# Kernel optimization log

Measured on AMD Instinct MI355X. Metric: run time of the kernel, lower is better.

The kernel has to match this reference:

```python
import jax, jax.numpy as jnp
import numpy as np

N_NODES = 50000
N_GRAPHS = 512
EPS = 1e-5


def _ln(x, g, b):
    mu = jnp.mean(x, axis=-1, keepdims=True)
    var = jnp.var(x, axis=-1, keepdims=True)
    return (x - mu) * jax.lax.rsqrt(var + EPS) * g + b


def _sage(x, src, dst, wl, wr, bl):
    # mean-aggregate neighbor features: messages x[src] -> dst
    s = jax.ops.segment_sum(x[src], dst, num_segments=N_NODES)
    cnt = jax.ops.segment_sum(jnp.ones((src.shape[0],), x.dtype), dst, num_segments=N_NODES)
    agg = s / jnp.maximum(cnt, 1.0)[:, None]
    # PyG SAGEConv: lin_l(agg) + lin_r(x), bias only on lin_l
    return agg @ wl + bl + x @ wr


def setup_inputs() -> dict:
    key = jax.random.key(0)
    ks = jax.random.split(key, 16)
    C, H, NC, E = 128, 128, 2, 800000
    inp = {
        'x': jax.random.normal(ks[0], (N_NODES, C), jnp.float32),
        'edge_index': jax.random.randint(ks[1], (2, E), 0, N_NODES, jnp.int32),
        'batch': jnp.sort(jax.random.randint(ks[2], (N_NODES,), 0, N_GRAPHS, jnp.int32)),
    }
    def w(k, shape):
        return jax.random.normal(k, shape, jnp.float32) * 0.05
    inp.update({
        'w1l': w(ks[3], (C, H)), 'w1r': w(ks[4], (C, H)), 'b1': jnp.zeros((H,), jnp.float32),
        'g1': jnp.ones((H,), jnp.float32), 'be1': jnp.zeros((H,), jnp.float32),
        'w2l': w(ks[5], (H, H)), 'w2r': w(ks[6], (H, H)), 'b2': jnp.zeros((H,), jnp.float32),
        'g2': jnp.ones((H,), jnp.float32), 'be2': jnp.zeros((H,), jnp.float32),
        'w3l': w(ks[7], (H, H)), 'w3r': w(ks[8], (H, H)), 'b3': jnp.zeros((H,), jnp.float32),
        'g3': jnp.ones((H,), jnp.float32), 'be3': jnp.zeros((H,), jnp.float32),
        'wc': w(ks[9], (H, NC)), 'bc': jnp.zeros((NC,), jnp.float32),
    })
    return inp


def reference(x, edge_index, batch, w1l, w1r, b1, g1, be1, w2l, w2r, b2, g2, be2,
              w3l, w3r, b3, g3, be3, wc, bc):
    src, dst = edge_index[0], edge_index[1]
    # eval mode: dropout is identity
    h1 = _ln(jax.nn.relu(_sage(x, src, dst, w1l, w1r, b1)), g1, be1)
    h2 = _ln(jax.nn.relu(_sage(h1, src, dst, w2l, w2r, b2)) + h1, g2, be2)
    h3 = _ln(h2 + jax.nn.relu(_sage(h2, src, dst, w3l, w3r, b3)), g3, be3)
    # global mean pool over graphs
    s = jax.ops.segment_sum(h3, batch, num_segments=N_GRAPHS)
    cnt = jax.ops.segment_sum(jnp.ones((h3.shape[0],), h3.dtype), batch, num_segments=N_GRAPHS)
    avg = s / jnp.maximum(cnt, 1.0)[:, None]
    out = avg @ wc + bc
    return (out, h3, avg)
```

## Files before the change

kernel.cpp:

```cpp
#include <hip/hip_runtime.h>

#define NND 50000
#define NE  800000
#define CF  128
#define NGR 512
#define DCAP 64

typedef __bf16 bf16;
typedef __bf16 bf16x2 __attribute__((ext_vector_type(2)));
typedef __bf16 bf16x4 __attribute__((ext_vector_type(4)));
typedef __bf16 bf16x8 __attribute__((ext_vector_type(8)));
typedef float  f32x4  __attribute__((ext_vector_type(4)));

__device__ __forceinline__ int swz(int n, int k) {
  return n * 256 + (((k >> 3) ^ (n & 31)) << 3) + (k & 7);
}

__global__ __launch_bounds__(256) void conv_k(const float* __restrict__ x,
                                              bf16* __restrict__ xb,
                                              const float* __restrict__ w1l, const float* __restrict__ w1r,
                                              const float* __restrict__ w2l, const float* __restrict__ w2r,
                                              const float* __restrict__ w3l, const float* __restrict__ w3r,
                                              bf16* __restrict__ wb,
                                              const int* __restrict__ batch,
                                              int* __restrict__ gs,
                                              int* __restrict__ cnt) {
  int t = blockIdx.x * 256 + threadIdx.x;
  if (t < (NND * CF / 4)) {
    f32x4 v = ((const f32x4*)x)[t];
    bf16x4 o;
    o[0] = (bf16)v[0]; o[1] = (bf16)v[1]; o[2] = (bf16)v[2]; o[3] = (bf16)v[3];
    ((bf16x4*)xb)[t] = o;
  }
  if (t < 49152) {
    int m = t >> 13, w = t & 8191;
    const float* src = (m == 0) ? w1l : (m == 1) ? w1r : (m == 2) ? w2l
                     : (m == 3) ? w2r : (m == 4) ? w3l : w3r;
    float2 v = *(const float2*)(src + w * 2);
    bf16x2 o;
    o[0] = (bf16)v.x; o[1] = (bf16)v.y;
    ((bf16x2*)wb)[t] = o;
  }
  if (t < NND) {
    cnt[t] = 0;
    int b = batch[t];
    if (t == 0) {
      for (int g = 0; g <= b; g++) gs[g] = 0;
    } else {
      int pb = batch[t - 1];
      for (int g = pb + 1; g <= b; g++) gs[g] = t;
    }
    if (t == NND - 1) {
      for (int g = b + 1; g <= NGR; g++) gs[g] = NND;
    }
  }
}

__global__ __launch_bounds__(256) void fill_k(const int* __restrict__ src,
                                              const int* __restrict__ dst,
                                              int* __restrict__ cnt,
                                              unsigned short* __restrict__ csr) {
  int r  = blockIdx.x & 7;
  int lo = r * 6250, hi = lo + 6250;
  int base = (blockIdx.x >> 3) * 2048;
  int end  = min(base + 2048, NE);
  for (int e = base + threadIdx.x; e < end; e += 256) {
    int d = dst[e];
    if (d >= lo && d < hi) {
      int p = atomicAdd(&cnt[d], 1);
      if (p < DCAP) csr[d * DCAP + p] = (unsigned short)src[e];
    }
  }
}

__global__ __launch_bounds__(256) void agg_k(const bf16* __restrict__ xin,
                                             const int* __restrict__ cnt,
                                             const unsigned short* __restrict__ csr,
                                             bf16* __restrict__ aggout) {
  int wid  = (blockIdx.x * 256 + threadIdx.x) >> 6;
  int lane = threadIdx.x & 63;
  if (wid >= NND) return;
  int sub = lane >> 4;
  int c8  = (lane & 15) * 8;
  int deg = min(cnt[wid], DCAP);
  int ebase = wid * DCAP;
  float a[8] = {};
  for (int e = 0; e < deg; e += 16) {
    int   s[4];
    float m[4];
#pragma unroll
    for (int u = 0; u < 4; u++) {
      int i = e + u * 4 + sub;
      s[u] = csr[ebase + ((i < deg) ? i : 0)];
      m[u] = (i < deg) ? 1.f : 0.f;
    }
    bf16x8 v[4];
#pragma unroll
    for (int u = 0; u < 4; u++) v[u] = *(const bf16x8*)(xin + s[u] * 128 + c8);
#pragma unroll
    for (int u = 0; u < 4; u++)
#pragma unroll
      for (int j = 0; j < 8; j++) a[j] += m[u] * (float)v[u][j];
  }
#pragma unroll
  for (int j = 0; j < 8; j++) {
    a[j] += __shfl_xor(a[j], 16);
    a[j] += __shfl_xor(a[j], 32);
  }
  if (sub == 0) {
    float inv = 1.0f / fmaxf((float)deg, 1.0f);
    bf16x8 o;
#pragma unroll
    for (int j = 0; j < 8; j++) o[j] = (bf16)(a[j] * inv);
    *(bf16x8*)(aggout + wid * 128 + c8) = o;
  }
}

template <typename TO>
__global__ __launch_bounds__(256, 2) void gemm_k(
    const bf16* __restrict__ aggp, const bf16* __restrict__ prev,
    const bf16* __restrict__ wl, const bf16* __restrict__ wr,
    const float* __restrict__ bias, const float* __restrict__ gamma,
    const float* __restrict__ beta, TO* __restrict__ outp, int addres) {
  __shared__ bf16 bt[128 * 256];
  int tid = threadIdx.x;
  for (int e = tid; e < 128 * 64; e += 256) {
    int k  = e >> 6;
    int n2 = (e & 63) << 1;
    {
      bf16x2 v = *(const bf16x2*)(wl + k * 128 + n2);
      bt[swz(n2, k)]     = v[0];
      bt[swz(n2 + 1, k)] = v[1];
    }
    {
      bf16x2 v = *(const bf16x2*)(wr + k * 128 + n2);
      bt[swz(n2, k + 128)]     = v[0];
      bt[swz(n2 + 1, k + 128)] = v[1];
    }
  }
  __syncthreads();

  int wave = tid >> 6, lane = tid & 63;
  int q = lane >> 4, r = lane & 15;
  int wrow = blockIdx.x * 128 + wave * 32;

  int arow[2];
#pragma unroll
  for (int rt = 0; rt < 2; rt++) {
    int ar = wrow + rt * 16 + r;
    arow[rt] = (ar < NND) ? ar : (NND - 1);
  }

  f32x4 acc[2][8] = {};

#pragma unroll
  for (int kk = 0; kk < 8; kk++) {
    int kof = kk * 32 + q * 8;
    bf16x8 af[2];
#pragma unroll
    for (int rt = 0; rt < 2; rt++) {
      const bf16* ap = (kk < 4) ? (aggp + arow[rt] * 128 + kof)
                                : (prev + arow[rt] * 128 + (kof - 128));
      af[rt] = *(const bf16x8*)ap;
    }
#pragma unroll
    for (int t = 0; t < 8; t++) {
      int n = t * 16 + r;
      bf16x8 bfrag = *(const bf16x8*)&bt[n * 256 + (((kof >> 3) ^ (n & 31)) << 3)];
#pragma unroll
      for (int rt = 0; rt < 2; rt++)
        acc[rt][t] = __builtin_amdgcn_mfma_f32_16x16x32_bf16(af[rt], bfrag, acc[rt][t], 0, 0, 0);
    }
  }

  float biasf[8], gf[8], bef[8];
#pragma unroll
  for (int t = 0; t < 8; t++) {
    int c = t * 16 + r;
    biasf[t] = bias[c];
    gf[t]    = gamma[c];
    bef[t]   = beta[c];
  }

#pragma unroll
  for (int rt = 0; rt < 2; rt++) {
#pragma unroll
    for (int reg = 0; reg < 4; reg++) {
      int row = wrow + rt * 16 + q * 4 + reg;
      int rr  = (row < NND) ? row : (NND - 1);
      const bf16* prow = prev + rr * 128;
      float vals[8];
      float s = 0.f, s2 = 0.f;
#pragma unroll
      for (int t = 0; t < 8; t++) {
        float v = acc[rt][t][reg] + biasf[t];
        v = fmaxf(v, 0.f);
        if (addres) v += (float)prow[t * 16 + r];
        vals[t] = v;
        s += v;
        s2 += v * v;
      }
#pragma unroll
      for (int m = 1; m < 16; m <<= 1) {
        s  += __shfl_xor(s, m);
        s2 += __shfl_xor(s2, m);
      }
      float mean = s * (1.f / 128.f);
      float var  = fmaxf(s2 * (1.f / 128.f) - mean * mean, 0.f);
      float rstd = rsqrtf(var + 1e-5f);
      if (row < NND) {
        TO* orow = outp + row * 128;
#pragma unroll
        for (int t = 0; t < 8; t++)
          orow[t * 16 + r] = (TO)((vals[t] - mean) * rstd * gf[t] + bef[t]);
      }
    }
  }
}

__global__ __launch_bounds__(256) void poolhead_k(
    const float* __restrict__ h3, const int* __restrict__ gs,
    const float* __restrict__ wc, const float* __restrict__ bc,
    float* __restrict__ outv, float* __restrict__ avgv) {
  int g = blockIdx.x;
  int s = gs[g], epos = gs[g + 1];
  int tid = threadIdx.x;
  int wave = tid >> 6, lane = tid & 63;
  float a0 = 0.f, a1 = 0.f;
  for (int row = s + wave; row < epos; row += 4) {
    float2 v = *(const float2*)(h3 + row * 128 + 2 * lane);
    a0 += v.x; a1 += v.y;
  }
  __shared__ float red[4][128];
  red[wave][2 * lane]     = a0;
  red[wave][2 * lane + 1] = a1;
  __syncthreads();
  __shared__ float sp[4];
  if (tid < 128) {
    float t4  = red[0][tid] + red[1][tid] + red[2][tid] + red[3][tid];
    float inv = 1.f / fmaxf((float)(epos - s), 1.f);
    float avg = t4 * inv;
    avgv[g * 128 + tid] = avg;
    float p0 = avg * wc[tid * 2 + 0];
    float p1 = avg * wc[tid * 2 + 1];
#pragma unroll
    for (int m = 1; m < 64; m <<= 1) {
      p0 += __shfl_xor(p0, m);
      p1 += __shfl_xor(p1, m);
    }
    if ((tid & 63) == 0) {
      sp[(tid >> 6) * 2]     = p0;
      sp[(tid >> 6) * 2 + 1] = p1;
    }
  }
  __syncthreads();
  if (tid == 0) {
    outv[g * 2 + 0] = sp[0] + sp[2] + bc[0];
    outv[g * 2 + 1] = sp[1] + sp[3] + bc[1];
  }
}

extern "C" void kernel_launch(void* const* d_in, const int* in_sizes, int n_in,
                              void* d_out, int out_size, void* d_ws, size_t ws_size,
                              hipStream_t stream) {
  const float* x   = (const float*)d_in[0];
  const int* ei    = (const int*)d_in[1];
  const int* batch = (const int*)d_in[2];
  const float* w1l = (const float*)d_in[3],  *w1r = (const float*)d_in[4];
  const float* b1  = (const float*)d_in[5],  *g1  = (const float*)d_in[6],  *be1 = (const float*)d_in[7];
  const float* w2l = (const float*)d_in[8],  *w2r = (const float*)d_in[9];
  const float* b2  = (const float*)d_in[10], *g2  = (const float*)d_in[11], *be2 = (const float*)d_in[12];
  const float* w3l = (const float*)d_in[13], *w3r = (const float*)d_in[14];
  const float* b3  = (const float*)d_in[15], *g3  = (const float*)d_in[16], *be3 = (const float*)d_in[17];
  const float* wc  = (const float*)d_in[18], *bc  = (const float*)d_in[19];
  const int* srcv = ei;
  const int* dstv = ei + NE;

  char* base = (char*)d_ws;
  int*            cnt  = (int*)(base + 0);
  int*            gs   = (int*)(base + 200064);
  bf16*           wb   = (bf16*)(base + 202752);
  unsigned short* csr  = (unsigned short*)(base + 399360);
  bf16*           agg  = (bf16*)(base + 6799360);
  bf16*           h1   = (bf16*)(base + 19599360);
  bf16*           h2xb = (bf16*)(base + 32399360);

  bf16* wb1l = wb,          *wb1r = wb + 16384;
  bf16* wb2l = wb + 32768,  *wb2r = wb + 49152;
  bf16* wb3l = wb + 65536,  *wb3r = wb + 81920;

  float* outv = (float*)d_out;
  float* h3   = outv + 1024;
  float* avgv = outv + 1024 + NND * CF;

  conv_k<<<6250, 256, 0, stream>>>(x, h2xb, w1l, w1r, w2l, w2r, w3l, w3r, wb, batch, gs, cnt);
  fill_k<<<3128, 256, 0, stream>>>(srcv, dstv, cnt, csr);

  agg_k<<<12500, 256, 0, stream>>>(h2xb, cnt, csr, agg);
  gemm_k<bf16><<<391, 256, 0, stream>>>(agg, h2xb, wb1l, wb1r, b1, g1, be1, h1, 0);
  agg_k<<<12500, 256, 0, stream>>>(h1, cnt, csr, agg);
  gemm_k<bf16><<<391, 256, 0, stream>>>(agg, h1, wb2l, wb2r, b2, g2, be2, h2xb, 1);
  agg_k<<<12500, 256, 0, stream>>>(h2xb, cnt, csr, agg);
  gemm_k<float><<<391, 256, 0, stream>>>(agg, h2xb, wb3l, wb3r, b3, g3, be3, h3, 1);
  poolhead_k<<<NGR, 256, 0, stream>>>(h3, gs, wc, bc, outv, avgv);
}
```

Measured before the change: 313.7 us.

## Fuse global mean pooling into final GEMM epilogue and halve fill chunk size

The final GEMM+LayerNorm kernel now accumulates per-graph sums of h3 directly in its epilogue, using register partials for the first graph, shared-memory atomics for nearby graphs and global atomics otherwise. This replaces the pooling kernel's second read of the 25 MB fp32 h3 with a small head kernel that reads the pooled sums. Separately, the CSR fill kernel uses 1024-edge chunks with twice the blocks and loads src unconditionally. The pooling adds atomics, an extra batch lookup per row and extra shared-memory syncs to the GEMM epilogue, and makes the summation order nondeterministic.

```diff
diff --git a/kernel.cpp b/kernel.cpp
--- a/kernel.cpp
+++ b/kernel.cpp
@@ -24,7 +24,8 @@
                                               bf16* __restrict__ wb,
                                               const int* __restrict__ batch,
                                               int* __restrict__ gs,
-                                              int* __restrict__ cnt) {
+                                              int* __restrict__ cnt,
+                                              float* __restrict__ pool) {
   int t = blockIdx.x * 256 + threadIdx.x;
   if (t < (NND * CF / 4)) {
     f32x4 v = ((const f32x4*)x)[t];
@@ -41,6 +42,7 @@
     o[0] = (bf16)v.x; o[1] = (bf16)v.y;
     ((bf16x2*)wb)[t] = o;
   }
+  if (t < NGR * CF) pool[t] = 0.f;
   if (t < NND) {
     cnt[t] = 0;
     int b = batch[t];
@@ -62,13 +64,14 @@
                                               unsigned short* __restrict__ csr) {
   int r  = blockIdx.x & 7;
   int lo = r * 6250, hi = lo + 6250;
-  int base = (blockIdx.x >> 3) * 2048;
-  int end  = min(base + 2048, NE);
+  int base = (blockIdx.x >> 3) * 1024;
+  int end  = min(base + 1024, NE);
   for (int e = base + threadIdx.x; e < end; e += 256) {
     int d = dst[e];
+    int s = src[e];
     if (d >= lo && d < hi) {
       int p = atomicAdd(&cnt[d], 1);
-      if (p < DCAP) csr[d * DCAP + p] = (unsigned short)src[e];
+      if (p < DCAP) csr[d * DCAP + p] = (unsigned short)s;
     }
   }
 }
@@ -116,12 +119,13 @@
   }
 }
 
-template <typename TO>
+template <typename TO, bool POOL>
 __global__ __launch_bounds__(256, 2) void gemm_k(
     const bf16* __restrict__ aggp, const bf16* __restrict__ prev,
     const bf16* __restrict__ wl, const bf16* __restrict__ wr,
     const float* __restrict__ bias, const float* __restrict__ gamma,
-    const float* __restrict__ beta, TO* __restrict__ outp, int addres) {
+    const float* __restrict__ beta, TO* __restrict__ outp, int addres,
+    const int* __restrict__ batch, float* __restrict__ pool) {
   __shared__ bf16 bt[128 * 256];
   int tid = threadIdx.x;
   for (int e = tid; e < 128 * 64; e += 256) {
@@ -173,6 +177,19 @@
     }
   }
 
+  float* lp = (float*)bt;
+  int g0base = 0;
+  float pacc[8];
+  int g0l = -1;
+  if (POOL) {
+    __syncthreads();
+    for (int idx = tid; idx < 8 * 128; idx += 256) lp[idx] = 0.f;
+    g0base = batch[blockIdx.x * 128];
+#pragma unroll
+    for (int t = 0; t < 8; t++) pacc[t] = 0.f;
+    __syncthreads();
+  }
+
   float biasf[8], gf[8], bef[8];
 #pragma unroll
   for (int t = 0; t < 8; t++) {
@@ -210,51 +227,72 @@
       float rstd = rsqrtf(var + 1e-5f);
       if (row < NND) {
         TO* orow = outp + row * 128;
-#pragma unroll
-        for (int t = 0; t < 8; t++)
-          orow[t * 16 + r] = (TO)((vals[t] - mean) * rstd * gf[t] + bef[t]);
+        int grow = 0; bool same = true;
+        if (POOL) {
+          grow = batch[row];
+          if (g0l < 0) g0l = grow;
+          same = (grow == g0l);
+        }
+#pragma unroll
+        for (int t = 0; t < 8; t++) {
+          float o = (vals[t] - mean) * rstd * gf[t] + bef[t];
+          orow[t * 16 + r] = (TO)o;
+          if (POOL) {
+            if (same) {
+              pacc[t] += o;
+            } else {
+              int gi = grow - g0base;
+              if (gi < 8) atomicAdd(&lp[gi * 128 + t * 16 + r], o);
+              else        atomicAdd(&pool[grow * 128 + t * 16 + r], o);
+            }
+          }
+        }
       }
     }
   }
-}
-
-__global__ __launch_bounds__(256) void poolhead_k(
-    const float* __restrict__ h3, const int* __restrict__ gs,
-    const float* __restrict__ wc, const float* __restrict__ bc,
-    float* __restrict__ outv, float* __restrict__ avgv) {
-  int g = blockIdx.x;
-  int s = gs[g], epos = gs[g + 1];
-  int tid = threadIdx.x;
-  int wave = tid >> 6, lane = tid & 63;
-  float a0 = 0.f, a1 = 0.f;
-  for (int row = s + wave; row < epos; row += 4) {
-    float2 v = *(const float2*)(h3 + row * 128 + 2 * lane);
-    a0 += v.x; a1 += v.y;
-  }
-  __shared__ float red[4][128];
-  red[wave][2 * lane]     = a0;
-  red[wave][2 * lane + 1] = a1;
+
+  if (POOL) {
+    if (g0l >= 0) {
+      int gi = g0l - g0base;
+#pragma unroll
+      for (int t = 0; t < 8; t++) {
+        if (gi < 8) atomicAdd(&lp[gi * 128 + t * 16 + r], pacc[t]);
+        else        atomicAdd(&pool[g0l * 128 + t * 16 + r], pacc[t]);
+      }
+    }
+    __syncthreads();
+    for (int idx = tid; idx < 8 * 128; idx += 256) {
+      float v = lp[idx];
+      if (v != 0.f) atomicAdd(&pool[(g0base + (idx >> 7)) * 128 + (idx & 127)], v);
+    }
+  }
+}
+
+__global__ __launch_bounds__(128) void head_k(const float* __restrict__ pool,
+                                              const int* __restrict__ gs,
+                                              const float* __restrict__ wc,
+                                              const float* __restrict__ bc,
+                                              float* __restrict__ outv,
+                                              float* __restrict__ avgv) {
+  int g = blockIdx.x, f = threadIdx.x;
+  int n = gs[g + 1] - gs[g];
+  float inv = 1.f / fmaxf((float)n, 1.f);
+  float avg = pool[g * 128 + f] * inv;
+  avgv[g * 128 + f] = avg;
+  float p0 = avg * wc[f * 2 + 0];
+  float p1 = avg * wc[f * 2 + 1];
+#pragma unroll
+  for (int m = 1; m < 64; m <<= 1) {
+    p0 += __shfl_xor(p0, m);
+    p1 += __shfl_xor(p1, m);
+  }
+  __shared__ float sp[4];
+  if ((f & 63) == 0) {
+    sp[(f >> 6) * 2]     = p0;
+    sp[(f >> 6) * 2 + 1] = p1;
+  }
   __syncthreads();
-  __shared__ float sp[4];
-  if (tid < 128) {
-    float t4  = red[0][tid] + red[1][tid] + red[2][tid] + red[3][tid];
-    float inv = 1.f / fmaxf((float)(epos - s), 1.f);
-    float avg = t4 * inv;
-    avgv[g * 128 + tid] = avg;
-    float p0 = avg * wc[tid * 2 + 0];
-    float p1 = avg * wc[tid * 2 + 1];
-#pragma unroll
-    for (int m = 1; m < 64; m <<= 1) {
-      p0 += __shfl_xor(p0, m);
-      p1 += __shfl_xor(p1, m);
-    }
-    if ((tid & 63) == 0) {
-      sp[(tid >> 6) * 2]     = p0;
-      sp[(tid >> 6) * 2 + 1] = p1;
-    }
-  }
-  __syncthreads();
-  if (tid == 0) {
+  if (f == 0) {
     outv[g * 2 + 0] = sp[0] + sp[2] + bc[0];
     outv[g * 2 + 1] = sp[1] + sp[3] + bc[1];
   }
@@ -284,6 +322,7 @@
   bf16*           agg  = (bf16*)(base + 6799360);
   bf16*           h1   = (bf16*)(base + 19599360);
   bf16*           h2xb = (bf16*)(base + 32399360);
+  float*          pool = (float*)(base + 45199360);
 
   bf16* wb1l = wb,          *wb1r = wb + 16384;
   bf16* wb2l = wb + 32768,  *wb2r = wb + 49152;
@@ -293,14 +332,14 @@
   float* h3   = outv + 1024;
   float* avgv = outv + 1024 + NND * CF;
 
-  conv_k<<<6250, 256, 0, stream>>>(x, h2xb, w1l, w1r, w2l, w2r, w3l, w3r, wb, batch, gs, cnt);
-  fill_k<<<3128, 256, 0, stream>>>(srcv, dstv, cnt, csr);
+  conv_k<<<6250, 256, 0, stream>>>(x, h2xb, w1l, w1r, w2l, w2r, w3l, w3r, wb, batch, gs, cnt, pool);
+  fill_k<<<6256, 256, 0, stream>>>(srcv, dstv, cnt, csr);
 
   agg_k<<<12500, 256, 0, stream>>>(h2xb, cnt, csr, agg);
-  gemm_k<bf16><<<391, 256, 0, stream>>>(agg, h2xb, wb1l, wb1r, b1, g1, be1, h1, 0);
+  gemm_k<bf16, false><<<391, 256, 0, stream>>>(agg, h2xb, wb1l, wb1r, b1, g1, be1, h1, 0, nullptr, nullptr);
   agg_k<<<12500, 256, 0, stream>>>(h1, cnt, csr, agg);
-  gemm_k<bf16><<<391, 256, 0, stream>>>(agg, h1, wb2l, wb2r, b2, g2, be2, h2xb, 1);
+  gemm_k<bf16, false><<<391, 256, 0, stream>>>(agg, h1, wb2l, wb2r, b2, g2, be2, h2xb, 1, nullptr, nullptr);
   agg_k<<<12500, 256, 0, stream>>>(h2xb, cnt, csr, agg);
-  gemm_k<float><<<391, 256, 0, stream>>>(agg, h2xb, wb3l, wb3r, b3, g3, be3, h3, 1);
-  poolhead_k<<<NGR, 256, 0, stream>>>(h3, gs, wc, bc, outv, avgv);
-}
+  gemm_k<float, true><<<391, 256, 0, stream>>>(agg, h2xb, wb3l, wb3r, b3, g3, be3, h3, 1, batch, pool);
+  head_k<<<NGR, 128, 0, stream>>>(pool, gs, wc, bc, outv, avgv);
+}
```

Measured after the change: 316.7 us. Within noise of the previous version (+0.9%).
